# Optimization experiments

Measured on AMD Instinct MI355X. Metric: run time of the kernel, lower is better.

The kernel has to match this reference:

```python
import jax, jax.numpy as jnp
import numpy as np

HEIGHT = 10
IN_DIM = 256
OUT_DIM = 16
BATCH = 65536


def _and_weight(height):
    # Fixed +/-1 tree-structured routing matrix [leaf_nodes, int_nodes]
    int_nodes = 2 ** height - 1
    leaf = 2 ** height
    w = np.zeros((leaf, int_nodes), dtype=np.float32)
    for i in range(height):
        num = 2 ** i
        start = num - 1
        for j in range(start, start + num):
            rb = leaf // num * (j - start)
            rm = rb + leaf // (2 * num)
            re = rb + leaf // num
            w[rb:rm, j] = 1.0
            w[rm:re, j] = -1.0
    return jnp.asarray(w)


def setup_inputs() -> dict:
    key = jax.random.key(0)
    k0, k1, k2, k3 = jax.random.split(key, 4)
    int_nodes = 2 ** HEIGHT - 1
    leaf = 2 ** HEIGHT
    return {
        "x": jax.random.normal(k0, (BATCH, IN_DIM), jnp.float32),
        "W_pred": jax.random.normal(k1, (int_nodes, IN_DIM), jnp.float32) / np.float32(np.sqrt(IN_DIM)),
        "b_pred": jnp.zeros((int_nodes,), jnp.float32),
        "W_or": jax.random.normal(k2, (OUT_DIM, leaf), jnp.float32) / np.float32(np.sqrt(leaf)),
        "action_stds": jax.random.normal(k3, (OUT_DIM, leaf), jnp.float32),
    }


def reference(x, W_pred, b_pred, W_or, action_stds):
    # predicate linear: [B, int_nodes]
    pred_z = x @ W_pred.T + b_pred
    # ScaleBinarizer1 (STE): scale = mean |z| per sample, binarize to {0, fac}
    fac = jax.lax.stop_gradient(jnp.mean(jnp.abs(pred_z), axis=-1, keepdims=True))
    hard = jnp.where(pred_z >= 0, fac, jnp.zeros_like(fac))
    pred_bin = pred_z + jax.lax.stop_gradient(hard - pred_z)  # straight-through
    pred_a = 2.0 * pred_bin - fac  # +/- fac (sign of pred_z scaled)
    # fixed tree AND layer: [B, leaf]
    W_and = _and_weight(HEIGHT)
    and_z = pred_a @ W_and.T
    and_a = jax.nn.softmax(and_z, axis=-1)
    # Sparser1 (STE): hard one-hot of the argmax leaf
    onehot = jax.nn.one_hot(jnp.argmax(and_a, axis=-1), and_a.shape[-1], dtype=and_a.dtype)
    and_a = and_a + jax.lax.stop_gradient(onehot - and_a)
    # OR layer + softmax over classes
    or_z = and_a @ W_or.T  # [B, out_dim]
    out = jax.nn.softmax(or_z, axis=-1)
    # per-action std: sum over leaves of and_a * action_stds, clamped
    std = jnp.clip(jnp.einsum("bl,ol->bo", and_a, action_stds), -20.0, 2.0)
    return out, std
```

## Files before the change

kernel.cpp:

```cpp
#include <hip/hip_runtime.h>


#define BATCH   65536
#define IN_DIM  256
#define NLEVEL  10
#define NLEAF   1024
#define OUT_DIM 16
#define EPS_TIE 1e-3f

#define DPP_QUAD_XOR1   0xB1
#define DPP_QUAD_XOR2   0x4E
#define DPP_HALF_MIRROR 0x141

template <int CTRL>
__device__ __forceinline__ float dpp_xfer(float v) {
    return __int_as_float(__builtin_amdgcn_update_dpp(
        0, __float_as_int(v), CTRL, 0xf, 0xf, true));
}

__device__ __forceinline__ float group8_sum(float v) {
    v += dpp_xfer<DPP_QUAD_XOR1>(v);
    v += dpp_xfer<DPP_QUAD_XOR2>(v);
    v += dpp_xfer<DPP_HALF_MIRROR>(v);
    return v;
}
__device__ __forceinline__ float group8_max(float v) {
    v = fmaxf(v, dpp_xfer<DPP_QUAD_XOR1>(v));
    v = fmaxf(v, dpp_xfer<DPP_QUAD_XOR2>(v));
    v = fmaxf(v, dpp_xfer<DPP_HALF_MIRROR>(v));
    return v;
}

__device__ __forceinline__ int tree_sign_f64(
    float4 x0, float4 x1, float4 x2, float4 x3,
    float4 x4, float4 x5, float4 x6, float4 x7,
    const float* wrow, float bias, int l)
{
    double A0 = 0.0, A1 = 0.0, A2 = 0.0, A3 = 0.0;
#define ACC64(K, XV)                                                        \
    {                                                                       \
        float4 w = *reinterpret_cast<const float4*>(wrow + (K)*32 + l * 4); \
        A0 += (double)XV.x * (double)w.x; A1 += (double)XV.y * (double)w.y; \
        A2 += (double)XV.z * (double)w.z; A3 += (double)XV.w * (double)w.w; \
    }
    ACC64(0, x0) ACC64(1, x1) ACC64(2, x2) ACC64(3, x3)
    ACC64(4, x4) ACC64(5, x5) ACC64(6, x6) ACC64(7, x7)
#undef ACC64
    double Z = (A0 + A1) + (A2 + A3);
    #pragma unroll
    for (int off = 4; off > 0; off >>= 1)
        Z += __shfl_xor(Z, off, 64);
    Z += (double)bias;
    return (Z < 0.0) ? 1 : 0;
}

__global__ __launch_bounds__(256, 3) void dgt_kernel(
    const float* __restrict__ x,
    const float* __restrict__ W_pred,
    const float* __restrict__ b_pred,
    const float* __restrict__ W_or,
    const float* __restrict__ a_std,
    float* __restrict__ out)
{
    const int lane = threadIdx.x & 63;
    const int wid  = threadIdx.x >> 6;
    const int l    = lane & 7;
    const int g    = lane >> 3;
    const int sample = blockIdx.x * 32 + wid * 8 + g;

    const float* xrow = x + (size_t)sample * IN_DIM;
    float4 x0 = *reinterpret_cast<const float4*>(xrow +   0 + l * 4);
    float4 x1 = *reinterpret_cast<const float4*>(xrow +  32 + l * 4);
    float4 x2 = *reinterpret_cast<const float4*>(xrow +  64 + l * 4);
    float4 x3 = *reinterpret_cast<const float4*>(xrow +  96 + l * 4);
    float4 x4 = *reinterpret_cast<const float4*>(xrow + 128 + l * 4);
    float4 x5 = *reinterpret_cast<const float4*>(xrow + 160 + l * 4);
    float4 x6 = *reinterpret_cast<const float4*>(xrow + 192 + l * 4);
    float4 x7 = *reinterpret_cast<const float4*>(xrow + 224 + l * 4);

    int node = 0, pos = 0;
    float bcur = b_pred[0];
    const float* wrow = W_pred;

    #pragma unroll
    for (int lvl = 0; lvl < NLEVEL; ++lvl) {
        float4 w0 = *reinterpret_cast<const float4*>(wrow +   0 + l * 4);
        float4 w1 = *reinterpret_cast<const float4*>(wrow +  32 + l * 4);
        float4 w2 = *reinterpret_cast<const float4*>(wrow +  64 + l * 4);
        float4 w3 = *reinterpret_cast<const float4*>(wrow +  96 + l * 4);
        float4 w4 = *reinterpret_cast<const float4*>(wrow + 128 + l * 4);
        float4 w5 = *reinterpret_cast<const float4*>(wrow + 160 + l * 4);
        float4 w6 = *reinterpret_cast<const float4*>(wrow + 192 + l * 4);
        float4 w7 = *reinterpret_cast<const float4*>(wrow + 224 + l * 4);

        float bL = 0.f, bR = 0.f;
        if (lvl < NLEVEL - 1) {
            bL = b_pred[2 * node + 1];
            bR = b_pred[2 * node + 2];
        }

        float a0, a1, a2, a3;
        a0  = x0.x * w0.x; a1  = x0.y * w0.y; a2  = x0.z * w0.z; a3  = x0.w * w0.w;
        a0 += x1.x * w1.x; a1 += x1.y * w1.y; a2 += x1.z * w1.z; a3 += x1.w * w1.w;
        a0 += x2.x * w2.x; a1 += x2.y * w2.y; a2 += x2.z * w2.z; a3 += x2.w * w2.w;
        a0 += x3.x * w3.x; a1 += x3.y * w3.y; a2 += x3.z * w3.z; a3 += x3.w * w3.w;
        a0 += x4.x * w4.x; a1 += x4.y * w4.y; a2 += x4.z * w4.z; a3 += x4.w * w4.w;
        a0 += x5.x * w5.x; a1 += x5.y * w5.y; a2 += x5.z * w5.z; a3 += x5.w * w5.w;
        a0 += x6.x * w6.x; a1 += x6.y * w6.y; a2 += x6.z * w6.z; a3 += x6.w * w6.w;
        a0 += x7.x * w7.x; a1 += x7.y * w7.y; a2 += x7.z * w7.z; a3 += x7.w * w7.w;
        float z = group8_sum((a0 + a1) + (a2 + a3)) + bcur;

        int right;
        if (__builtin_expect(fabsf(z) >= EPS_TIE, 1))
            right = (z < 0.f) ? 1 : 0;
        else
            right = tree_sign_f64(x0, x1, x2, x3, x4, x5, x6, x7,
                                  wrow, bcur, l);

        pos  = 2 * pos + right;
        node = 2 * node + 1 + right;
        if (lvl < NLEVEL - 1) {
            bcur = right ? bR : bL;
            wrow = W_pred + (size_t)node * IN_DIM;
        }
    }
    const int leaf = pos;

    float zx = W_or[(size_t)(2 * l)     * NLEAF + leaf];
    float zy = W_or[(size_t)(2 * l + 1) * NLEAF + leaf];
    float m  = group8_max(fmaxf(zx, zy));
    float ex = __expf(zx - m), ey = __expf(zy - m);
    float s  = group8_sum(ex + ey);
    *reinterpret_cast<float2*>(out + (size_t)sample * OUT_DIM + 2 * l) =
        make_float2(ex / s, ey / s);

    float dx = a_std[(size_t)(2 * l)     * NLEAF + leaf];
    float dy = a_std[(size_t)(2 * l + 1) * NLEAF + leaf];
    *reinterpret_cast<float2*>(out + (size_t)BATCH * OUT_DIM
                               + (size_t)sample * OUT_DIM + 2 * l) =
        make_float2(fminf(fmaxf(dx, -20.f), 2.f),
                    fminf(fmaxf(dy, -20.f), 2.f));
}

extern "C" void kernel_launch(void* const* d_in, const int* in_sizes, int n_in,
                              void* d_out, int out_size, void* d_ws, size_t ws_size,
                              hipStream_t stream) {
    const float* x      = (const float*)d_in[0];
    const float* W_pred = (const float*)d_in[1];
    const float* b_pred = (const float*)d_in[2];
    const float* W_or   = (const float*)d_in[3];
    const float* a_std  = (const float*)d_in[4];
    float* out = (float*)d_out;

    hipLaunchKernelGGL(dgt_kernel, dim3(BATCH / 32), dim3(256), 0, stream,
                       x, W_pred, b_pred, W_or, a_std, out);
}
```

Measured before the change: 37.36 us.

## Use bf16-packed predicate weights with fp64 fallback for near-zero decisions

Adds a prep kernel that rounds W_pred to bf16 and packs pairs into a workspace, then walks the tree using those packed weights. This halves the weight bytes gathered per tree level, and the tie threshold is widened so that near-zero decisions still fall back to an exact fp64 dot product against the fp32 weights. Each lane now reads 8 contiguous x values per chunk instead of 4. The cost is an extra kernel launch plus more frequent fp64 fallbacks, and correctness still depends on the bf16 error staying below the threshold.

```diff
diff --git a/kernel.cpp b/kernel.cpp
--- a/kernel.cpp
+++ b/kernel.cpp
@@ -1,4 +1,5 @@
 #include <hip/hip_runtime.h>
+#include <stdint.h>
 
 
 #define BATCH   65536
@@ -6,7 +7,8 @@
 #define NLEVEL  10
 #define NLEAF   1024
 #define OUT_DIM 16
-#define EPS_TIE 1e-3f
+#define EPS_TIE 0.02f
+#define WB_U32  (1023 * 128)
 
 #define DPP_QUAD_XOR1   0xB1
 #define DPP_QUAD_XOR2   0x4E
@@ -17,7 +19,6 @@
     return __int_as_float(__builtin_amdgcn_update_dpp(
         0, __float_as_int(v), CTRL, 0xf, 0xf, true));
 }
-
 __device__ __forceinline__ float group8_sum(float v) {
     v += dpp_xfer<DPP_QUAD_XOR1>(v);
     v += dpp_xfer<DPP_QUAD_XOR2>(v);
@@ -31,7 +32,132 @@
     return v;
 }
 
+__device__ __forceinline__ float blo(uint32_t u) { return __uint_as_float(u << 16); }
+__device__ __forceinline__ float bhi(uint32_t u) { return __uint_as_float(u & 0xffff0000u); }
+
+__global__ __launch_bounds__(256) void dgt_prep(
+    const float* __restrict__ W, uint32_t* __restrict__ Wb)
+{
+    int i = blockIdx.x * 256 + threadIdx.x;
+    if (i < WB_U32) {
+        uint32_t ua = __float_as_uint(W[2 * i]);
+        uint32_t ub = __float_as_uint(W[2 * i + 1]);
+        uint32_t ra = (ua + 0x7fffu + ((ua >> 16) & 1u)) >> 16;
+        uint32_t rb = (ub + 0x7fffu + ((ub >> 16) & 1u)) >> 16;
+        Wb[i] = ra | (rb << 16);
+    }
+}
+
 __device__ __forceinline__ int tree_sign_f64(
+    float4 x0a, float4 x0b, float4 x1a, float4 x1b,
+    float4 x2a, float4 x2b, float4 x3a, float4 x3b,
+    const float* wrow, float bias, int l)
+{
+    double A0 = 0.0, A1 = 0.0, A2 = 0.0, A3 = 0.0;
+#define ACC64(K, XA, XB)                                                     \
+    {                                                                        \
+        float4 wa = *reinterpret_cast<const float4*>(wrow + (K)*64 + l * 8); \
+        float4 wb = *reinterpret_cast<const float4*>(wrow + (K)*64 + l * 8 + 4); \
+        A0 += (double)XA.x * (double)wa.x; A1 += (double)XA.y * (double)wa.y; \
+        A2 += (double)XA.z * (double)wa.z; A3 += (double)XA.w * (double)wa.w; \
+        A0 += (double)XB.x * (double)wb.x; A1 += (double)XB.y * (double)wb.y; \
+        A2 += (double)XB.z * (double)wb.z; A3 += (double)XB.w * (double)wb.w; \
+    }
+    ACC64(0, x0a, x0b) ACC64(1, x1a, x1b) ACC64(2, x2a, x2b) ACC64(3, x3a, x3b)
+#undef ACC64
+    double Z = (A0 + A1) + (A2 + A3);
+    #pragma unroll
+    for (int off = 4; off > 0; off >>= 1)
+        Z += __shfl_xor(Z, off, 64);
+    Z += (double)bias;
+    return (Z < 0.0) ? 1 : 0;
+}
+
+__global__ __launch_bounds__(256, 2) void dgt_bf16(
+    const float* __restrict__ x,
+    const uint32_t* __restrict__ Wb,
+    const float* __restrict__ W_pred,
+    const float* __restrict__ b_pred,
+    const float* __restrict__ W_or,
+    const float* __restrict__ a_std,
+    float* __restrict__ out)
+{
+    const int lane = threadIdx.x & 63;
+    const int wid  = threadIdx.x >> 6;
+    const int l    = lane & 7;
+    const int g    = lane >> 3;
+    const int sample = blockIdx.x * 32 + wid * 8 + g;
+
+    const float* xrow = x + (size_t)sample * IN_DIM;
+    float4 x0a = *reinterpret_cast<const float4*>(xrow +   0 + l * 8);
+    float4 x0b = *reinterpret_cast<const float4*>(xrow +   4 + l * 8);
+    float4 x1a = *reinterpret_cast<const float4*>(xrow +  64 + l * 8);
+    float4 x1b = *reinterpret_cast<const float4*>(xrow +  68 + l * 8);
+    float4 x2a = *reinterpret_cast<const float4*>(xrow + 128 + l * 8);
+    float4 x2b = *reinterpret_cast<const float4*>(xrow + 132 + l * 8);
+    float4 x3a = *reinterpret_cast<const float4*>(xrow + 192 + l * 8);
+    float4 x3b = *reinterpret_cast<const float4*>(xrow + 196 + l * 8);
+
+    int node = 0, pos = 0;
+    float bcur = b_pred[0];
+
+    #pragma unroll
+    for (int lvl = 0; lvl < NLEVEL; ++lvl) {
+        const uint32_t* wb = Wb + (size_t)node * 128;
+        uint4 u0 = *reinterpret_cast<const uint4*>(wb +  0 + l * 4);
+        uint4 u1 = *reinterpret_cast<const uint4*>(wb + 32 + l * 4);
+        uint4 u2 = *reinterpret_cast<const uint4*>(wb + 64 + l * 4);
+        uint4 u3 = *reinterpret_cast<const uint4*>(wb + 96 + l * 4);
+
+        float bL = 0.f, bR = 0.f;
+        if (lvl < NLEVEL - 1) {
+            bL = b_pred[2 * node + 1];
+            bR = b_pred[2 * node + 2];
+        }
+
+        float a0 = 0.f, a1 = 0.f, a2 = 0.f, a3 = 0.f;
+#define ACCB(U, XA, XB)                                     \
+        a0 += XA.x * blo(U.x); a1 += XA.y * bhi(U.x);       \
+        a2 += XA.z * blo(U.y); a3 += XA.w * bhi(U.y);       \
+        a0 += XB.x * blo(U.z); a1 += XB.y * bhi(U.z);       \
+        a2 += XB.z * blo(U.w); a3 += XB.w * bhi(U.w);
+        ACCB(u0, x0a, x0b)
+        ACCB(u1, x1a, x1b)
+        ACCB(u2, x2a, x2b)
+        ACCB(u3, x3a, x3b)
+#undef ACCB
+        float z = group8_sum((a0 + a1) + (a2 + a3)) + bcur;
+
+        int right;
+        if (__builtin_expect(fabsf(z) >= EPS_TIE, 1))
+            right = (z < 0.f) ? 1 : 0;
+        else
+            right = tree_sign_f64(x0a, x0b, x1a, x1b, x2a, x2b, x3a, x3b,
+                                  W_pred + (size_t)node * IN_DIM, bcur, l);
+
+        pos  = 2 * pos + right;
+        node = 2 * node + 1 + right;
+        if (lvl < NLEVEL - 1) bcur = right ? bR : bL;
+    }
+    const int leaf = pos;
+
+    float zx = W_or[(size_t)(2 * l)     * NLEAF + leaf];
+    float zy = W_or[(size_t)(2 * l + 1) * NLEAF + leaf];
+    float m  = group8_max(fmaxf(zx, zy));
+    float ex = __expf(zx - m), ey = __expf(zy - m);
+    float s  = group8_sum(ex + ey);
+    *reinterpret_cast<float2*>(out + (size_t)sample * OUT_DIM + 2 * l) =
+        make_float2(ex / s, ey / s);
+
+    float dx = a_std[(size_t)(2 * l)     * NLEAF + leaf];
+    float dy = a_std[(size_t)(2 * l + 1) * NLEAF + leaf];
+    *reinterpret_cast<float2*>(out + (size_t)BATCH * OUT_DIM
+                               + (size_t)sample * OUT_DIM + 2 * l) =
+        make_float2(fminf(fmaxf(dx, -20.f), 2.f),
+                    fminf(fmaxf(dy, -20.f), 2.f));
+}
+
+__device__ __forceinline__ int tree_sign_f64_r8(
     float4 x0, float4 x1, float4 x2, float4 x3,
     float4 x4, float4 x5, float4 x6, float4 x7,
     const float* wrow, float bias, int l)
@@ -54,7 +180,7 @@
     return (Z < 0.0) ? 1 : 0;
 }
 
-__global__ __launch_bounds__(256, 3) void dgt_kernel(
+__global__ __launch_bounds__(256, 2) void dgt_f32(
     const float* __restrict__ x,
     const float* __restrict__ W_pred,
     const float* __restrict__ b_pred,
@@ -111,11 +237,11 @@
         float z = group8_sum((a0 + a1) + (a2 + a3)) + bcur;
 
         int right;
-        if (__builtin_expect(fabsf(z) >= EPS_TIE, 1))
+        if (__builtin_expect(fabsf(z) >= 1e-3f, 1))
             right = (z < 0.f) ? 1 : 0;
         else
-            right = tree_sign_f64(x0, x1, x2, x3, x4, x5, x6, x7,
-                                  wrow, bcur, l);
+            right = tree_sign_f64_r8(x0, x1, x2, x3, x4, x5, x6, x7,
+                                     wrow, bcur, l);
 
         pos  = 2 * pos + right;
         node = 2 * node + 1 + right;
@@ -152,6 +278,14 @@
     const float* a_std  = (const float*)d_in[4];
     float* out = (float*)d_out;
 
-    hipLaunchKernelGGL(dgt_kernel, dim3(BATCH / 32), dim3(256), 0, stream,
-                       x, W_pred, b_pred, W_or, a_std, out);
-}
+    if (ws_size >= (size_t)WB_U32 * 4) {
+        uint32_t* Wb = (uint32_t*)d_ws;
+        hipLaunchKernelGGL(dgt_prep, dim3((WB_U32 + 255) / 256), dim3(256),
+                           0, stream, W_pred, Wb);
+        hipLaunchKernelGGL(dgt_bf16, dim3(BATCH / 32), dim3(256), 0, stream,
+                           x, Wb, W_pred, b_pred, W_or, a_std, out);
+    } else {
+        hipLaunchKernelGGL(dgt_f32, dim3(BATCH / 32), dim3(256), 0, stream,
+                           x, W_pred, b_pred, W_or, a_std, out);
+    }
+}
```

Result: slower. 43.09 us (+15.3%).
